# Performance work log

Measured on AMD Instinct MI355X. Metric: run time of the kernel, lower is better.

Reference implementation:

```python
import jax, jax.numpy as jnp
import numpy as np
from jax import lax


def setup_inputs() -> dict:
    key = jax.random.key(0)
    ks = jax.random.split(key, 8)
    B, S, V, E, H, O = 64, 200, 50000, 300, 512, 5
    return {
        "x": jax.random.randint(ks[0], (B, S), 0, V),
        "emb": jax.random.normal(ks[1], (V, E), dtype=jnp.float32),
        "W_ih": jax.random.normal(ks[2], (4 * H, E), dtype=jnp.float32) * 0.05,
        "W_hh": jax.random.normal(ks[3], (4 * H, H), dtype=jnp.float32) * 0.05,
        "b_ih": jax.random.normal(ks[4], (4 * H,), dtype=jnp.float32) * 0.05,
        "b_hh": jax.random.normal(ks[5], (4 * H,), dtype=jnp.float32) * 0.05,
        "W_fc": jax.random.normal(ks[6], (O, H), dtype=jnp.float32) * 0.05,
        "b_fc": jax.random.normal(ks[7], (O,), dtype=jnp.float32) * 0.05,
        "batch_size": B,
    }


def reference(x, emb, W_ih, W_hh, b_ih, b_hh, W_fc, b_fc, batch_size):
    H = W_hh.shape[1]
    B = x.shape[0]
    vec = jnp.transpose(emb[x], (1, 0, 2))  # [S, B, E] (time-major, as nn.LSTM)
    b = b_ih + b_hh  # [4H]

    def step(carry, xt):
        h, c = carry
        gates = xt @ W_ih.T + h @ W_hh.T + b  # [B, 4H]
        i, f, g, o = jnp.split(gates, 4, axis=-1)  # PyTorch gate order i,f,g,o
        i = jax.nn.sigmoid(i)
        f = jax.nn.sigmoid(f)
        g = jnp.tanh(g)
        o = jax.nn.sigmoid(o)
        c = f * c + i * g
        h = o * jnp.tanh(c)
        return (h, c), None

    h0 = jnp.zeros((B, H), dtype=vec.dtype)
    c0 = jnp.zeros((B, H), dtype=vec.dtype)
    (h_final, _), _ = lax.scan(step, (h0, c0), vec)
    logits = h_final @ W_fc.T + b_fc  # [B, O]
    return jax.nn.softmax(logits, axis=-1)
```

## Files before the change

kernel.cpp:

```cpp
#include <hip/hip_runtime.h>

#define TPB   256
#define NWG   256
#define SEQL  200
#define BATCH 64
#define EDIM  300
#define HDIM  512
#define ODIM  5
#define NROW  (4*HDIM)

#define GROUPS 8
#define GCUS   32
#define GB     8
#define UNITS  16
#define KSLC   32

#define H_WORDS  4096
#define EX_OFF   4096
#define EX_RSTR  137
#define EX_BSTR  17
#define EMB_OFF  (EX_OFF + 64*EX_RSTR)
#define LDS_BYTES 83968

#define HT_GROUP 4096
#define HT_PAR   (GROUPS * HT_GROUP)
#define HT_TOTAL (2 * HT_PAR)
#define HT_BYTES (HT_TOTAL * 8)

#define ESTR 308
#define PRE_LDS_BYTES (BATCH * ESTR * 4)

#define GATES_FLOATS ((size_t)SEQL * NROW * BATCH)

__device__ __forceinline__ float fast_sigmoid(float x) {
    return 1.0f / (1.0f + __expf(-x));
}
__device__ __forceinline__ float fast_tanh(float x) {
    return 2.0f / (1.0f + __expf(-2.0f * x)) - 1.0f;
}

extern "C" __global__ void __launch_bounds__(256, 1)
lstm_pre(const int* __restrict__ x, const float* __restrict__ emb,
         const float* __restrict__ W_ih, float* __restrict__ gates)
{
    extern __shared__ float embs[];
    const int tid = threadIdx.x;
    const int s   = blockIdx.x >> 3;
    const int rb  = blockIdx.x & 7;

    for (int i = tid; i < BATCH * 75; i += 256) {
        int b = i / 75, jj = i - b * 75;
        int row = x[b * SEQL + s];
        float4 v = ((const float4*)(emb + (size_t)row * EDIM))[jj];
        *(float4*)&embs[b * ESTR + 4 * jj] = v;
    }
    __syncthreads();

    const int bi = tid >> 5;
    const int ri = tid & 31;
    const int row0 = rb * 256 + ri * 8;
    const float* wp = W_ih + (size_t)row0 * EDIM;

    float acc[8][8];
#pragma unroll
    for (int a = 0; a < 8; a++)
#pragma unroll
        for (int b = 0; b < 8; b++) acc[a][b] = 0.0f;

    for (int t2 = 0; t2 < 75; t2++) {
        float4 w[8], e[8];
#pragma unroll
        for (int rr = 0; rr < 8; rr++)
            w[rr] = *(const float4*)(wp + rr * EDIM + 4 * t2);
#pragma unroll
        for (int bb = 0; bb < 8; bb++)
            e[bb] = *(const float4*)&embs[(bi * 8 + bb) * ESTR + 4 * t2];
#pragma unroll
        for (int rr = 0; rr < 8; rr++)
#pragma unroll
            for (int bb = 0; bb < 8; bb++) {
                acc[rr][bb] = fmaf(w[rr].x, e[bb].x, acc[rr][bb]);
                acc[rr][bb] = fmaf(w[rr].y, e[bb].y, acc[rr][bb]);
                acc[rr][bb] = fmaf(w[rr].z, e[bb].z, acc[rr][bb]);
                acc[rr][bb] = fmaf(w[rr].w, e[bb].w, acc[rr][bb]);
            }
    }
#pragma unroll
    for (int rr = 0; rr < 8; rr++) {
        float* dst = gates + (((size_t)s * 8 + bi) * NROW + row0 + rr) * 8;
        *(float4*)dst       = make_float4(acc[rr][0], acc[rr][1], acc[rr][2], acc[rr][3]);
        *(float4*)(dst + 4) = make_float4(acc[rr][4], acc[rr][5], acc[rr][6], acc[rr][7]);
    }
}

extern "C" __global__ void __launch_bounds__(TPB, 1)
lstm_persist(const int* __restrict__ x, const float* __restrict__ emb,
             const float* __restrict__ W_ih, const float* __restrict__ W_hh,
             const float* __restrict__ b_ih, const float* __restrict__ b_hh,
             const float* __restrict__ gates,
             unsigned long long* __restrict__ htag)
{
    extern __shared__ float lds[];
    const int tid = threadIdx.x;
    const int g   = blockIdx.x & 7;
    const int j   = blockIdx.x >> 3;
    const bool pre = (gates != nullptr);

    const int rq = tid & 15;
    const int kh = tid >> 4;

    float4 w4[4][8];
#pragma unroll
    for (int p = 0; p < 4; p++) {
        const int r = 4 * rq + p;
        const size_t R = (size_t)((r >> 4) * HDIM + UNITS * j + (r & 15));
        const float* wp = W_hh + R * HDIM + KSLC * kh;
#pragma unroll
        for (int kq = 0; kq < 8; kq++) w4[p][kq] = *(const float4*)(wp + 4 * kq);
    }
#pragma unroll
    for (int p = 0; p < 4; p++)
#pragma unroll
        for (int kq = 0; kq < 8; kq++)
            asm volatile("" : "+v"(w4[p][kq].x), "+v"(w4[p][kq].y),
                             "+v"(w4[p][kq].z), "+v"(w4[p][kq].w));

    const int cu = tid >> 3;
    const int cbb = tid & 7;
    float bias4[4];
#pragma unroll
    for (int gt = 0; gt < 4; gt++) {
        int R = gt * HDIM + UNITS * j + (cu & 15);
        bias4[gt] = b_ih[R] + b_hh[R];
    }
    float c_reg = 0.0f;

    const int sw = 4 * (kh & 1);

    unsigned long long* const T0 = htag + (size_t)g * HT_GROUP;
    unsigned long long* const T1 = htag + HT_PAR + (size_t)g * HT_GROUP;

    __syncthreads();

    for (int s = 0; s < SEQL; s++) {
        const unsigned long long* Tin = (s & 1) ? T1 : T0;
        unsigned long long*       Tout = (s & 1) ? T0 : T1;

        float gp[4] = {0.f, 0.f, 0.f, 0.f};
        if (pre && tid < 128) {
            const float* gbase = gates + (((size_t)s * 8 + g) * NROW + UNITS * j) * 8;
#pragma unroll
            for (int gt = 0; gt < 4; gt++)
                gp[gt] = __builtin_nontemporal_load(gbase + (size_t)gt * (HDIM * 8) + tid);
        }

        float acc[4][8];
#pragma unroll
        for (int p = 0; p < 4; p++)
#pragma unroll
            for (int b = 0; b < 8; b++) acc[p][b] = 0.f;

        if (!pre) {
            for (int i = tid; i < EDIM * GB; i += TPB) {
                int e = i >> 3, b = i & 7;
                int row = x[(GB * g + b) * SEQL + s];
                lds[EMB_OFF + e * 8 + b] = emb[(size_t)row * EDIM + e];
            }
            __syncthreads();
            if (kh < 15) {
                for (int e = 20 * kh; e < 20 * kh + 20; e++) {
                    float4 e0 = *(const float4*)&lds[EMB_OFF + e * 8];
                    float4 e1 = *(const float4*)&lds[EMB_OFF + e * 8 + 4];
#pragma unroll
                    for (int p = 0; p < 4; p++) {
                        const int r = 4 * rq + p;
                        const size_t R = (size_t)((r >> 4) * HDIM + UNITS * j + (r & 15));
                        float wc = W_ih[R * EDIM + e];
                        acc[p][0] = fmaf(wc, e0.x, acc[p][0]);
                        acc[p][1] = fmaf(wc, e0.y, acc[p][1]);
                        acc[p][2] = fmaf(wc, e0.z, acc[p][2]);
                        acc[p][3] = fmaf(wc, e0.w, acc[p][3]);
                        acc[p][4] = fmaf(wc, e1.x, acc[p][4]);
                        acc[p][5] = fmaf(wc, e1.y, acc[p][5]);
                        acc[p][6] = fmaf(wc, e1.z, acc[p][6]);
                        acc[p][7] = fmaf(wc, e1.w, acc[p][7]);
                    }
                }
            }
            __syncthreads();
        }

        {
            const unsigned tag = (unsigned)s;
#pragma unroll
            for (int u = 0; u < 4; u++) {
                const int vi = 4 * tid + 1024 * u;
                unsigned long long d0, d1, d2, d3;
                for (;;) {
                    d0 = __hip_atomic_load(Tin + vi + 0, __ATOMIC_RELAXED, __HIP_MEMORY_SCOPE_AGENT);
                    d1 = __hip_atomic_load(Tin + vi + 1, __ATOMIC_RELAXED, __HIP_MEMORY_SCOPE_AGENT);
                    d2 = __hip_atomic_load(Tin + vi + 2, __ATOMIC_RELAXED, __HIP_MEMORY_SCOPE_AGENT);
                    d3 = __hip_atomic_load(Tin + vi + 3, __ATOMIC_RELAXED, __HIP_MEMORY_SCOPE_AGENT);
                    if ((unsigned)(d0 >> 32) == tag && (unsigned)(d1 >> 32) == tag &&
                        (unsigned)(d2 >> 32) == tag && (unsigned)(d3 >> 32) == tag)
                        break;
                    __builtin_amdgcn_s_sleep(1);
                }
                float4 hv;
                hv.x = __uint_as_float((unsigned)d0);
                hv.y = __uint_as_float((unsigned)d1);
                hv.z = __uint_as_float((unsigned)d2);
                hv.w = __uint_as_float((unsigned)d3);
                const int blk = tid + 256 * u;
                const int k = blk >> 1, hf = blk & 1;
                const int phys = 8 * k + 4 * (hf ^ ((k >> 5) & 1));
                *(float4*)&lds[phys] = hv;
            }
        }
        __syncthreads();

#pragma unroll
        for (int kq = 0; kq < 8; kq++) {
#pragma unroll
            for (int ki = 0; ki < 4; ki++) {
                const int kb = 256 * kh + 8 * (4 * kq + ki);
                float4 h0 = *(const float4*)&lds[kb + sw];
                float4 h1 = *(const float4*)&lds[kb + (4 - sw)];
#pragma unroll
                for (int p = 0; p < 4; p++) {
                    const float4 wv = w4[p][kq];
                    const float wc = ki == 0 ? wv.x : ki == 1 ? wv.y
                                   : ki == 2 ? wv.z : wv.w;
                    acc[p][0] = fmaf(wc, h0.x, acc[p][0]);
                    acc[p][1] = fmaf(wc, h0.y, acc[p][1]);
                    acc[p][2] = fmaf(wc, h0.z, acc[p][2]);
                    acc[p][3] = fmaf(wc, h0.w, acc[p][3]);
                    acc[p][4] = fmaf(wc, h1.x, acc[p][4]);
                    acc[p][5] = fmaf(wc, h1.y, acc[p][5]);
                    acc[p][6] = fmaf(wc, h1.z, acc[p][6]);
                    acc[p][7] = fmaf(wc, h1.w, acc[p][7]);
                }
            }
        }
        __syncthreads();

#pragma unroll
        for (int p = 0; p < 4; p++) {
            const int base = EX_OFF + (4 * rq + p) * EX_RSTR + kh;
#pragma unroll
            for (int b = 0; b < 8; b++)
                lds[base + b * EX_BSTR] = acc[p][b];
        }
        __syncthreads();

        if (tid < 128) {
            float gs[4];
#pragma unroll
            for (int gt = 0; gt < 4; gt++) {
                float sum = bias4[gt] + gp[gt];
                const int base = EX_OFF + (gt * 16 + cu) * EX_RSTR + cbb * EX_BSTR;
#pragma unroll
                for (int kk = 0; kk < 16; kk++) sum += lds[base + kk];
                gs[gt] = sum;
            }
            float iv = fast_sigmoid(gs[0]);
            float fv = fast_sigmoid(gs[1]);
            float gv = fast_tanh(gs[2]);
            float ov = fast_sigmoid(gs[3]);
            c_reg = fv * c_reg + iv * gv;
            float hv = ov * fast_tanh(c_reg);
            unsigned long long wword =
                ((unsigned long long)(unsigned)(s + 1) << 32) |
                (unsigned long long)__float_as_uint(hv);
            __hip_atomic_store(Tout + 128 * j + tid, wword,
                               __ATOMIC_RELAXED, __HIP_MEMORY_SCOPE_AGENT);
        }
    }
}

extern "C" __global__ void __launch_bounds__(320)
lstm_epilogue(const unsigned long long* __restrict__ htag,
              const float* __restrict__ W_fc, const float* __restrict__ b_fc,
              float* __restrict__ out)
{
    __shared__ float sl[ODIM * BATCH];
    const int t = threadIdx.x;
    {
        int o = t / BATCH, b = t - o * BATCH;
        const unsigned long long* hb = htag + (size_t)(b >> 3) * HT_GROUP;
        const int bc = b & 7;
        float acc = b_fc[o];
        const float4* wv = (const float4*)(W_fc + o * HDIM);
#pragma unroll 8
        for (int k4 = 0; k4 < HDIM / 4; k4++) {
            float4 w = wv[k4];
            const int k0 = 4 * k4;
            acc = fmaf(__uint_as_float((unsigned)hb[(k0 + 0) * 8 + bc]), w.x, acc);
            acc = fmaf(__uint_as_float((unsigned)hb[(k0 + 1) * 8 + bc]), w.y, acc);
            acc = fmaf(__uint_as_float((unsigned)hb[(k0 + 2) * 8 + bc]), w.z, acc);
            acc = fmaf(__uint_as_float((unsigned)hb[(k0 + 3) * 8 + bc]), w.w, acc);
        }
        sl[o * BATCH + b] = acc;
    }
    __syncthreads();
    if (t < BATCH) {
        float l0 = sl[t], l1 = sl[BATCH + t], l2 = sl[2 * BATCH + t];
        float l3 = sl[3 * BATCH + t], l4 = sl[4 * BATCH + t];
        float m = fmaxf(fmaxf(fmaxf(l0, l1), fmaxf(l2, l3)), l4);
        float e0 = __expf(l0 - m), e1 = __expf(l1 - m), e2 = __expf(l2 - m);
        float e3 = __expf(l3 - m), e4 = __expf(l4 - m);
        float inv = 1.0f / (e0 + e1 + e2 + e3 + e4);
        out[t * ODIM + 0] = e0 * inv;
        out[t * ODIM + 1] = e1 * inv;
        out[t * ODIM + 2] = e2 * inv;
        out[t * ODIM + 3] = e3 * inv;
        out[t * ODIM + 4] = e4 * inv;
    }
}

extern "C" void kernel_launch(void* const* d_in, const int* in_sizes, int n_in,
                              void* d_out, int out_size, void* d_ws, size_t ws_size,
                              hipStream_t stream)
{
    const int*   x    = (const int*)d_in[0];
    const float* emb  = (const float*)d_in[1];
    const float* W_ih = (const float*)d_in[2];
    const float* W_hh = (const float*)d_in[3];
    const float* b_ih = (const float*)d_in[4];
    const float* b_hh = (const float*)d_in[5];
    const float* W_fc = (const float*)d_in[6];
    const float* b_fc = (const float*)d_in[7];
    float* out = (float*)d_out;

    unsigned long long* htag = (unsigned long long*)d_ws;
    const size_t gates_bytes = GATES_FLOATS * sizeof(float);
    float* gates = nullptr;
    if (ws_size >= (size_t)HT_BYTES + gates_bytes)
        gates = (float*)((char*)d_ws + HT_BYTES);

    (void)hipMemsetAsync(htag, 0, HT_BYTES, stream);

    (void)hipFuncSetAttribute((const void*)lstm_persist,
                              hipFuncAttributeMaxDynamicSharedMemorySize, LDS_BYTES);
    if (gates) {
        (void)hipFuncSetAttribute((const void*)lstm_pre,
                                  hipFuncAttributeMaxDynamicSharedMemorySize, PRE_LDS_BYTES);
        lstm_pre<<<SEQL * 8, 256, PRE_LDS_BYTES, stream>>>(x, emb, W_ih, gates);
    }

    lstm_persist<<<NWG, TPB, LDS_BYTES, stream>>>(x, emb, W_ih, W_hh, b_ih, b_hh,
                                                  gates, htag);

    lstm_epilogue<<<1, 320, 0, stream>>>(htag, W_fc, b_fc, out);
}
```

Before: 1.746 ms.

## Split LSTM batch into 16 groups of 4 with two workgroups per CU

The persistent LSTM kernel now splits the batch into 16 groups of 4 sequences instead of 8 groups of 8. It launches 512 workgroups with launch bounds allowing two per CU, which halves per-step FMA work and LDS use per workgroup. Each wave now loads only the h slice it consumes, so the barrier after the h gather becomes a compiler fence, and the barrier after the matvec is dropped in favour of one at the end of the step. The pre-GEMM output layout and the epilogue are re-indexed to match. The change trades more cross-workgroup polling traffic and register pressure under two-per-CU occupancy for shorter per-step latency on the serial recurrence.

```diff
diff --git a/kernel.cpp b/kernel.cpp
--- a/kernel.cpp
+++ b/kernel.cpp
@@ -1,7 +1,7 @@
 #include <hip/hip_runtime.h>
 
 #define TPB   256
-#define NWG   256
+#define NWG   512
 #define SEQL  200
 #define BATCH 64
 #define EDIM  300
@@ -9,23 +9,21 @@
 #define ODIM  5
 #define NROW  (4*HDIM)
 
-#define GROUPS 8
+#define GROUPS 16
 #define GCUS   32
-#define GB     8
+#define GB     4
 #define UNITS  16
 #define KSLC   32
 
-#define H_WORDS  4096
-#define EX_OFF   4096
-#define EX_RSTR  137
+#define EX_OFF   2048
+#define EX_RSTR  69
 #define EX_BSTR  17
 #define EMB_OFF  (EX_OFF + 64*EX_RSTR)
-#define LDS_BYTES 83968
-
-#define HT_GROUP 4096
+#define LDS_BYTES 56320
+
+#define HT_GROUP 2048
 #define HT_PAR   (GROUPS * HT_GROUP)
-#define HT_TOTAL (2 * HT_PAR)
-#define HT_BYTES (HT_TOTAL * 8)
+#define HT_BYTES (2 * HT_PAR * 8)
 
 #define ESTR 308
 #define PRE_LDS_BYTES (BATCH * ESTR * 4)
@@ -85,15 +83,16 @@
                 acc[rr][bb] = fmaf(w[rr].w, e[bb].w, acc[rr][bb]);
             }
     }
+    float* dstA = gates + (size_t)(s * GROUPS + 2 * bi)     * 8192 + row0 * 4;
+    float* dstB = gates + (size_t)(s * GROUPS + 2 * bi + 1) * 8192 + row0 * 4;
 #pragma unroll
     for (int rr = 0; rr < 8; rr++) {
-        float* dst = gates + (((size_t)s * 8 + bi) * NROW + row0 + rr) * 8;
-        *(float4*)dst       = make_float4(acc[rr][0], acc[rr][1], acc[rr][2], acc[rr][3]);
-        *(float4*)(dst + 4) = make_float4(acc[rr][4], acc[rr][5], acc[rr][6], acc[rr][7]);
-    }
-}
-
-extern "C" __global__ void __launch_bounds__(TPB, 1)
+        *(float4*)(dstA + 4 * rr) = make_float4(acc[rr][0], acc[rr][1], acc[rr][2], acc[rr][3]);
+        *(float4*)(dstB + 4 * rr) = make_float4(acc[rr][4], acc[rr][5], acc[rr][6], acc[rr][7]);
+    }
+}
+
+extern "C" __global__ void __launch_bounds__(TPB, 2)
 lstm_persist(const int* __restrict__ x, const float* __restrict__ emb,
              const float* __restrict__ W_ih, const float* __restrict__ W_hh,
              const float* __restrict__ b_ih, const float* __restrict__ b_hh,
@@ -102,12 +101,14 @@
 {
     extern __shared__ float lds[];
     const int tid = threadIdx.x;
-    const int g   = blockIdx.x & 7;
-    const int j   = blockIdx.x >> 3;
+    const int g   = blockIdx.x & 15;
+    const int j   = blockIdx.x >> 4;
     const bool pre = (gates != nullptr);
 
     const int rq = tid & 15;
     const int kh = tid >> 4;
+    const int wv = tid >> 6;
+    const int ln = tid & 63;
 
     float4 w4[4][8];
 #pragma unroll
@@ -125,17 +126,17 @@
             asm volatile("" : "+v"(w4[p][kq].x), "+v"(w4[p][kq].y),
                              "+v"(w4[p][kq].z), "+v"(w4[p][kq].w));
 
-    const int cu = tid >> 3;
-    const int cbb = tid & 7;
+    const int uu = (tid & 63) >> 2;
+    const int cb = tid & 3;
     float bias4[4];
 #pragma unroll
     for (int gt = 0; gt < 4; gt++) {
-        int R = gt * HDIM + UNITS * j + (cu & 15);
+        int R = gt * HDIM + UNITS * j + uu;
         bias4[gt] = b_ih[R] + b_hh[R];
     }
     float c_reg = 0.0f;
 
-    const int sw = 4 * (kh & 1);
+    const int swz = (kh & 3) << 2;
 
     unsigned long long* const T0 = htag + (size_t)g * HT_GROUP;
     unsigned long long* const T1 = htag + HT_PAR + (size_t)g * HT_GROUP;
@@ -147,30 +148,29 @@
         unsigned long long*       Tout = (s & 1) ? T0 : T1;
 
         float gp[4] = {0.f, 0.f, 0.f, 0.f};
-        if (pre && tid < 128) {
-            const float* gbase = gates + (((size_t)s * 8 + g) * NROW + UNITS * j) * 8;
+        if (pre && tid < 64) {
+            const float* gbase = gates + (size_t)(s * GROUPS + g) * 8192 + 64 * j;
 #pragma unroll
             for (int gt = 0; gt < 4; gt++)
-                gp[gt] = __builtin_nontemporal_load(gbase + (size_t)gt * (HDIM * 8) + tid);
-        }
-
-        float acc[4][8];
+                gp[gt] = __builtin_nontemporal_load(gbase + gt * 2048 + tid);
+        }
+
+        float acc[4][4];
 #pragma unroll
         for (int p = 0; p < 4; p++)
 #pragma unroll
-            for (int b = 0; b < 8; b++) acc[p][b] = 0.f;
+            for (int b = 0; b < 4; b++) acc[p][b] = 0.f;
 
         if (!pre) {
             for (int i = tid; i < EDIM * GB; i += TPB) {
-                int e = i >> 3, b = i & 7;
+                int e = i >> 2, b = i & 3;
                 int row = x[(GB * g + b) * SEQL + s];
-                lds[EMB_OFF + e * 8 + b] = emb[(size_t)row * EDIM + e];
+                lds[EMB_OFF + i] = emb[(size_t)row * EDIM + e];
             }
             __syncthreads();
             if (kh < 15) {
                 for (int e = 20 * kh; e < 20 * kh + 20; e++) {
-                    float4 e0 = *(const float4*)&lds[EMB_OFF + e * 8];
-                    float4 e1 = *(const float4*)&lds[EMB_OFF + e * 8 + 4];
+                    float4 e0 = *(const float4*)&lds[EMB_OFF + 4 * e];
 #pragma unroll
                     for (int p = 0; p < 4; p++) {
                         const int r = 4 * rq + p;
@@ -180,10 +180,6 @@
                         acc[p][1] = fmaf(wc, e0.y, acc[p][1]);
                         acc[p][2] = fmaf(wc, e0.z, acc[p][2]);
                         acc[p][3] = fmaf(wc, e0.w, acc[p][3]);
-                        acc[p][4] = fmaf(wc, e1.x, acc[p][4]);
-                        acc[p][5] = fmaf(wc, e1.y, acc[p][5]);
-                        acc[p][6] = fmaf(wc, e1.z, acc[p][6]);
-                        acc[p][7] = fmaf(wc, e1.w, acc[p][7]);
                     }
                 }
             }
@@ -193,8 +189,9 @@
         {
             const unsigned tag = (unsigned)s;
 #pragma unroll
-            for (int u = 0; u < 4; u++) {
-                const int vi = 4 * tid + 1024 * u;
+            for (int rr = 0; rr < 2; rr++) {
+                const int k = 128 * wv + 64 * rr + ln;
+                const int vi = 4 * k;
                 unsigned long long d0, d1, d2, d3;
                 for (;;) {
                     d0 = __hip_atomic_load(Tin + vi + 0, __ATOMIC_RELAXED, __HIP_MEMORY_SCOPE_AGENT);
@@ -206,59 +203,51 @@
                         break;
                     __builtin_amdgcn_s_sleep(1);
                 }
+                const int phys = (4 * k) ^ (((k >> 5) & 3) << 2);
                 float4 hv;
                 hv.x = __uint_as_float((unsigned)d0);
                 hv.y = __uint_as_float((unsigned)d1);
                 hv.z = __uint_as_float((unsigned)d2);
                 hv.w = __uint_as_float((unsigned)d3);
-                const int blk = tid + 256 * u;
-                const int k = blk >> 1, hf = blk & 1;
-                const int phys = 8 * k + 4 * (hf ^ ((k >> 5) & 1));
                 *(float4*)&lds[phys] = hv;
             }
         }
-        __syncthreads();
+        asm volatile("" ::: "memory");
 
 #pragma unroll
         for (int kq = 0; kq < 8; kq++) {
 #pragma unroll
             for (int ki = 0; ki < 4; ki++) {
-                const int kb = 256 * kh + 8 * (4 * kq + ki);
-                float4 h0 = *(const float4*)&lds[kb + sw];
-                float4 h1 = *(const float4*)&lds[kb + (4 - sw)];
+                const int kidx = 4 * kq + ki;
+                const float4 h0 = *(const float4*)&lds[128 * kh + ((4 * kidx) ^ swz)];
 #pragma unroll
                 for (int p = 0; p < 4; p++) {
-                    const float4 wv = w4[p][kq];
-                    const float wc = ki == 0 ? wv.x : ki == 1 ? wv.y
-                                   : ki == 2 ? wv.z : wv.w;
+                    const float4 wvv = w4[p][kq];
+                    const float wc = ki == 0 ? wvv.x : ki == 1 ? wvv.y
+                                   : ki == 2 ? wvv.z : wvv.w;
                     acc[p][0] = fmaf(wc, h0.x, acc[p][0]);
                     acc[p][1] = fmaf(wc, h0.y, acc[p][1]);
                     acc[p][2] = fmaf(wc, h0.z, acc[p][2]);
                     acc[p][3] = fmaf(wc, h0.w, acc[p][3]);
-                    acc[p][4] = fmaf(wc, h1.x, acc[p][4]);
-                    acc[p][5] = fmaf(wc, h1.y, acc[p][5]);
-                    acc[p][6] = fmaf(wc, h1.z, acc[p][6]);
-                    acc[p][7] = fmaf(wc, h1.w, acc[p][7]);
                 }
             }
         }
-        __syncthreads();
 
 #pragma unroll
         for (int p = 0; p < 4; p++) {
             const int base = EX_OFF + (4 * rq + p) * EX_RSTR + kh;
 #pragma unroll
-            for (int b = 0; b < 8; b++)
+            for (int b = 0; b < 4; b++)
                 lds[base + b * EX_BSTR] = acc[p][b];
         }
         __syncthreads();
 
-        if (tid < 128) {
+        if (tid < 64) {
             float gs[4];
 #pragma unroll
             for (int gt = 0; gt < 4; gt++) {
                 float sum = bias4[gt] + gp[gt];
-                const int base = EX_OFF + (gt * 16 + cu) * EX_RSTR + cbb * EX_BSTR;
+                const int base = EX_OFF + (gt * 16 + uu) * EX_RSTR + cb * EX_BSTR;
 #pragma unroll
                 for (int kk = 0; kk < 16; kk++) sum += lds[base + kk];
                 gs[gt] = sum;
@@ -272,9 +261,10 @@
             unsigned long long wword =
                 ((unsigned long long)(unsigned)(s + 1) << 32) |
                 (unsigned long long)__float_as_uint(hv);
-            __hip_atomic_store(Tout + 128 * j + tid, wword,
+            __hip_atomic_store(Tout + 64 * j + tid, wword,
                                __ATOMIC_RELAXED, __HIP_MEMORY_SCOPE_AGENT);
         }
+        __syncthreads();
     }
 }
 
@@ -287,18 +277,18 @@
     const int t = threadIdx.x;
     {
         int o = t / BATCH, b = t - o * BATCH;
-        const unsigned long long* hb = htag + (size_t)(b >> 3) * HT_GROUP;
-        const int bc = b & 7;
+        const unsigned long long* hb = htag + (size_t)(b >> 2) * HT_GROUP;
+        const int bc = b & 3;
         float acc = b_fc[o];
         const float4* wv = (const float4*)(W_fc + o * HDIM);
 #pragma unroll 8
         for (int k4 = 0; k4 < HDIM / 4; k4++) {
             float4 w = wv[k4];
             const int k0 = 4 * k4;
-            acc = fmaf(__uint_as_float((unsigned)hb[(k0 + 0) * 8 + bc]), w.x, acc);
-            acc = fmaf(__uint_as_float((unsigned)hb[(k0 + 1) * 8 + bc]), w.y, acc);
-            acc = fmaf(__uint_as_float((unsigned)hb[(k0 + 2) * 8 + bc]), w.z, acc);
-            acc = fmaf(__uint_as_float((unsigned)hb[(k0 + 3) * 8 + bc]), w.w, acc);
+            acc = fmaf(__uint_as_float((unsigned)hb[(k0 + 0) * 4 + bc]), w.x, acc);
+            acc = fmaf(__uint_as_float((unsigned)hb[(k0 + 1) * 4 + bc]), w.y, acc);
+            acc = fmaf(__uint_as_float((unsigned)hb[(k0 + 2) * 4 + bc]), w.z, acc);
+            acc = fmaf(__uint_as_float((unsigned)hb[(k0 + 3) * 4 + bc]), w.w, acc);
         }
         sl[o * BATCH + b] = acc;
     }
```

New measurement: 1.732 ms. No clear change (-0.8%).
